# Optimization experiments

Hardware: AMD Instinct MI355X
Metric: run time of the kernel (lower is better)

The kernel has to match this reference:

```python
import jax, jax.numpy as jnp
import numpy as np

B, LQ, LK, D = 16, 1024, 4096, 256
SQRT_SCALE_INV = 0.25          # D ** -0.25, so scale = 1/sqrt(D)
HALF_BW = 128 // 2             # stripe_bandwdith // 2
NEG_INF = float('-inf')


def setup_inputs() -> dict:
    key = jax.random.key(0)
    k1, k2, k3, k4 = jax.random.split(key, 4)
    query = jax.random.normal(k1, (B, LQ, D), jnp.float32)
    key_t = jax.random.normal(k2, (B, LK, D), jnp.float32)
    value = jax.random.normal(k3, (B, LK, D), jnp.float32)
    # key lengths in [LK//2, LK]; masked_fill in torch requires max == LK
    key_lengths = jax.random.randint(k4, (B,), LK // 2, LK + 1).astype(jnp.int32)
    key_lengths = key_lengths.at[0].set(LK)
    query_lengths = jnp.full((B,), LQ, dtype=jnp.int32)  # full so no all-masked rows
    mask = jnp.arange(LK)[None, :] < key_lengths[:, None]  # [B, LK] bool, True = valid
    return {"query": query, "key": key_t, "value": value, "mask": mask,
            "query_lengths": query_lengths, "key_lengths": key_lengths}


def _stripe_mask(query_lengths, key_lengths, Lq, Lk):
    # band around line y = x * (key_len / query_len), per sample
    gx = jnp.arange(Lq, dtype=jnp.float32)[None, :, None]   # [1,Lq,1]
    gy = jnp.arange(Lk, dtype=jnp.float32)[None, None, :]   # [1,1,Lk]
    slope = (key_lengths.astype(jnp.float32) /
             query_lengths.astype(jnp.float32))[:, None, None]  # [B,1,1]
    center = gx * slope
    return (gy >= center - HALF_BW) & (gy <= center + HALF_BW)  # [B,Lq,Lk] bool


def reference(query, key, value, mask, query_lengths, key_lengths):
    # scores = (q * s) @ (k * s)^T  ==  (q @ k^T) * s^2
    scores = jnp.einsum('bqd,bkd->bqk', query, key) * (SQRT_SCALE_INV * SQRT_SCALE_INV)
    stripe = _stripe_mask(query_lengths, key_lengths, query.shape[1], key.shape[1])
    full_mask = mask[:, None, :] & stripe                    # padding AND stripe
    scores = jnp.where(full_mask, scores.astype(jnp.float32), NEG_INF)
    weight = jax.nn.softmax(scores, axis=-1).astype(query.dtype)
    # module applies no dropout (p=0) and returns (attn_weight, value)
    return (weight, value)
```

## Files before the change

### kernel.cpp

```cpp
#include <hip/hip_runtime.h>
#include <math.h>

constexpr int B_  = 16;
constexpr int LQ_ = 1024;
constexpr int LK_ = 4096;
constexpr int D_  = 256;
constexpr float HALF_BW_F = 64.0f;
constexpr float SCALE = 0.0625f;

typedef float  fx4    __attribute__((ext_vector_type(4)));
typedef short  bf16x8 __attribute__((ext_vector_type(8)));
typedef float  f32x4v __attribute__((ext_vector_type(4)));

constexpr int ROWS_PER_WAVE = 16;
constexpr int NUNIT = (B_ * LQ_) / ROWS_PER_WAVE;
constexpr int NXCD  = 8;
constexpr int UNIT_PER_XCD = NUNIT / NXCD;
constexpr int KSPAN = 192;
constexpr int NT    = 12;

__device__ __forceinline__ unsigned short f2bf(float f) {
    unsigned int u = __float_as_uint(f);
    return (unsigned short)((u + 0x7FFFu + ((u >> 16) & 1u)) >> 16);
}
__device__ __forceinline__ bf16x8 pack8(float4 a, float4 b) {
    bf16x8 r;
    r[0] = (short)f2bf(a.x); r[1] = (short)f2bf(a.y);
    r[2] = (short)f2bf(a.z); r[3] = (short)f2bf(a.w);
    r[4] = (short)f2bf(b.x); r[5] = (short)f2bf(b.y);
    r[6] = (short)f2bf(b.z); r[7] = (short)f2bf(b.w);
    return r;
}
__device__ __forceinline__ float grp16_max(float v) {
    #pragma unroll
    for (int off = 8; off > 0; off >>= 1)
        v = fmaxf(v, __shfl_xor(v, off, 64));
    return v;
}
__device__ __forceinline__ float grp16_sum(float v) {
    #pragma unroll
    for (int off = 8; off > 0; off >>= 1)
        v += __shfl_xor(v, off, 64);
    return v;
}

__global__ __launch_bounds__(64, 2) void fused_kernel(
    const float* __restrict__ Q, const float* __restrict__ K,
    const float* __restrict__ V,
    const int* __restrict__ qlen, const int* __restrict__ klen,
    float* __restrict__ Wout, float* __restrict__ Vout)
{
    const int Bid  = blockIdx.x;
    const int rb   = (Bid & (NXCD - 1)) * UNIT_PER_XCD + (Bid >> 3);
    const int lane = threadIdx.x;
    const int row0 = rb * ROWS_PER_WAVE;
    const int b    = row0 >> 10;
    const int qi0  = row0 & (LQ_ - 1);

    __shared__ float s_sc[ROWS_PER_WAVE][KSPAN];

    const int   key_len = klen[b];
    const float slope   = (float)key_len / (float)qlen[b];

    int lo_w = (int)ceilf((float)qi0 * slope - HALF_BW_F);
    if (lo_w < 0) lo_w = 0;
    int hi_w = (int)floorf((float)(qi0 + 15) * slope + HALF_BW_F);
    if (hi_w > key_len - 1) hi_w = key_len - 1;
    const int nt = (hi_w - lo_w) / 16 + 1;

    const int col = lane & 15;
    const int kg  = lane >> 4;

    const float* qb = Q + ((size_t)b * LQ_ + qi0 + col) * D_ + kg * 8;
    bf16x8 qf[8];
    #pragma unroll
    for (int kc = 0; kc < 8; ++kc) {
        const float4 u = *(const float4*)(qb + kc * 32);
        const float4 v = *(const float4*)(qb + kc * 32 + 4);
        qf[kc] = pack8(u, v);
    }

    const float* kb = K + (size_t)b * LK_ * D_ + kg * 8;
    f32x4v acc[NT];
    #pragma unroll
    for (int t = 0; t < NT; ++t) acc[t] = (f32x4v){0.f, 0.f, 0.f, 0.f};

    #pragma unroll
    for (int t = 0; t < NT; ++t) {
        if (t < nt) {
            const int key  = lo_w + t * 16 + col;
            const int keyc = (key <= hi_w) ? key : hi_w;
            const float* kp = kb + (size_t)keyc * D_;
            float4 u[8], w[8];
            #pragma unroll
            for (int kc = 0; kc < 8; ++kc) {
                u[kc] = *(const float4*)(kp + kc * 32);
                w[kc] = *(const float4*)(kp + kc * 32 + 4);
            }
            #pragma unroll
            for (int kc = 0; kc < 8; ++kc) {
                const bf16x8 kf = pack8(u[kc], w[kc]);
                acc[t] = __builtin_amdgcn_mfma_f32_16x16x32_bf16(qf[kc], kf, acc[t], 0, 0, 0);
            }
        }
    }

    #pragma unroll
    for (int r = 0; r < 4; ++r) {
        const int rg = kg * 4 + r;
        const float center = (float)(qi0 + rg) * slope;
        int klo = (int)ceilf(center - HALF_BW_F); if (klo < 0) klo = 0;
        int khi = (int)floorf(center + HALF_BW_F); if (khi > key_len - 1) khi = key_len - 1;

        float v[NT];
        #pragma unroll
        for (int t = 0; t < NT; ++t) {
            const int key = lo_w + t * 16 + col;
            v[t] = (t < nt && key >= klo && key <= khi) ? acc[t][r] * SCALE : -INFINITY;
        }
        float mx = v[0];
        #pragma unroll
        for (int t = 1; t < NT; ++t) mx = fmaxf(mx, v[t]);
        mx = grp16_max(mx);

        float e[NT], ssum = 0.f;
        #pragma unroll
        for (int t = 0; t < NT; ++t) { e[t] = __expf(v[t] - mx); ssum += e[t]; }
        ssum = grp16_sum(ssum);
        const float inv = 1.0f / ssum;

        #pragma unroll
        for (int t = 0; t < NT; ++t)
            if (t < nt) s_sc[rg][t * 16 + col] = e[t] * inv;
    }

    #pragma unroll
    for (int r = 0; r < 16; ++r) {
        const float center = (float)(qi0 + r) * slope;
        int klo = (int)ceilf(center - HALF_BW_F); if (klo < 0) klo = 0;
        int khi = (int)floorf(center + HALF_BW_F); if (khi > key_len - 1) khi = key_len - 1;
        const int s_lo = klo >> 8, s_hi = khi >> 8;
        float* base = Wout + (size_t)(row0 + r) * LK_;
        const float* sr = &s_sc[r][0];
        #pragma unroll
        for (int j = 0; j < 16; ++j) {
            const int c0 = (j * 64 + lane) * 4;
            float w[4] = {0.f, 0.f, 0.f, 0.f};
            if (j >= s_lo && j <= s_hi && c0 + 3 >= klo && c0 <= khi) {
                #pragma unroll
                for (int i = 0; i < 4; ++i) {
                    const int c = c0 + i;
                    if (c >= klo && c <= khi) w[i] = sr[c - lo_w];
                }
            }
            fx4 w4; w4.x = w[0]; w4.y = w[1]; w4.z = w[2]; w4.w = w[3];
            __builtin_nontemporal_store(w4, (fx4*)(base + c0));
        }
    }

    {
        const float* vs = V    + (size_t)row0 * 1024;
        float*       vd = Vout + (size_t)row0 * 1024;
        #pragma unroll
        for (int it = 0; it < 64; ++it) {
            const int o = (it * 64 + lane) * 4;
            fx4 t = __builtin_nontemporal_load((const fx4*)(vs + o));
            __builtin_nontemporal_store(t, (fx4*)(vd + o));
        }
    }
}

extern "C" void kernel_launch(void* const* d_in, const int* in_sizes, int n_in,
                              void* d_out, int out_size, void* d_ws, size_t ws_size,
                              hipStream_t stream) {
    const float* Q    = (const float*)d_in[0];
    const float* K    = (const float*)d_in[1];
    const float* V    = (const float*)d_in[2];
    const int*   qlen = (const int*)d_in[4];
    const int*   klen = (const int*)d_in[5];

    float* Wout = (float*)d_out;
    const size_t W_ELEMS = (size_t)B_ * LQ_ * LK_;
    float* Vout = Wout + W_ELEMS;

    fused_kernel<<<dim3(NUNIT), dim3(64), 0, stream>>>(
        Q, K, V, qlen, klen, Wout, Vout);
}
```

Baseline: 120.3 us.

## Split each 16-row unit across four waves with shared-memory softmax

Each block now has 256 threads instead of 64. The four waves each compute a third of the 12 key tiles of QK^T with MFMA and stage the raw scaled scores in shared memory. After a barrier, each wave runs the softmax and writes the weights for 4 of the 16 rows, and copies its own share of the V passthrough. The aim is more in-flight memory traffic per CU and less register pressure per wave than the single-wave-per-unit design. The cost is a block barrier, extra LDS traffic, and each wave reloading the same Q fragment.

```diff
diff --git a/kernel.cpp b/kernel.cpp
--- a/kernel.cpp
+++ b/kernel.cpp
@@ -12,12 +12,13 @@
 typedef short  bf16x8 __attribute__((ext_vector_type(8)));
 typedef float  f32x4v __attribute__((ext_vector_type(4)));
 
-constexpr int ROWS_PER_WAVE = 16;
-constexpr int NUNIT = (B_ * LQ_) / ROWS_PER_WAVE;
+constexpr int ROWS_PER_UNIT = 16;
+constexpr int NUNIT = (B_ * LQ_) / ROWS_PER_UNIT;
 constexpr int NXCD  = 8;
 constexpr int UNIT_PER_XCD = NUNIT / NXCD;
 constexpr int KSPAN = 192;
 constexpr int NT    = 12;
+constexpr int TPW   = 3;
 
 __device__ __forceinline__ unsigned short f2bf(float f) {
     unsigned int u = __float_as_uint(f);
@@ -31,33 +32,35 @@
     r[6] = (short)f2bf(b.z); r[7] = (short)f2bf(b.w);
     return r;
 }
-__device__ __forceinline__ float grp16_max(float v) {
+__device__ __forceinline__ float wave_max(float v) {
     #pragma unroll
-    for (int off = 8; off > 0; off >>= 1)
+    for (int off = 32; off > 0; off >>= 1)
         v = fmaxf(v, __shfl_xor(v, off, 64));
     return v;
 }
-__device__ __forceinline__ float grp16_sum(float v) {
+__device__ __forceinline__ float wave_sum(float v) {
     #pragma unroll
-    for (int off = 8; off > 0; off >>= 1)
+    for (int off = 32; off > 0; off >>= 1)
         v += __shfl_xor(v, off, 64);
     return v;
 }
 
-__global__ __launch_bounds__(64, 2) void fused_kernel(
+__global__ __launch_bounds__(256, 4) void fused_kernel(
     const float* __restrict__ Q, const float* __restrict__ K,
     const float* __restrict__ V,
     const int* __restrict__ qlen, const int* __restrict__ klen,
     float* __restrict__ Wout, float* __restrict__ Vout)
 {
     const int Bid  = blockIdx.x;
-    const int rb   = (Bid & (NXCD - 1)) * UNIT_PER_XCD + (Bid >> 3);
-    const int lane = threadIdx.x;
-    const int row0 = rb * ROWS_PER_WAVE;
+    const int unit = (Bid & (NXCD - 1)) * UNIT_PER_XCD + (Bid >> 3);
+    const int tid  = threadIdx.x;
+    const int lane = tid & 63;
+    const int wave = tid >> 6;
+    const int row0 = unit * ROWS_PER_UNIT;
     const int b    = row0 >> 10;
     const int qi0  = row0 & (LQ_ - 1);
 
-    __shared__ float s_sc[ROWS_PER_WAVE][KSPAN];
+    __shared__ float s_sc[ROWS_PER_UNIT][KSPAN];
 
     const int   key_len = klen[b];
     const float slope   = (float)key_len / (float)qlen[b];
@@ -81,12 +84,9 @@
     }
 
     const float* kb = K + (size_t)b * LK_ * D_ + kg * 8;
-    f32x4v acc[NT];
     #pragma unroll
-    for (int t = 0; t < NT; ++t) acc[t] = (f32x4v){0.f, 0.f, 0.f, 0.f};
-
-    #pragma unroll
-    for (int t = 0; t < NT; ++t) {
+    for (int s = 0; s < TPW; ++s) {
+        const int t = wave + 4 * s;
         if (t < nt) {
             const int key  = lo_w + t * 16 + col;
             const int keyc = (key <= hi_w) ? key : hi_w;
@@ -97,51 +97,47 @@
                 u[kc] = *(const float4*)(kp + kc * 32);
                 w[kc] = *(const float4*)(kp + kc * 32 + 4);
             }
+            f32x4v acc = (f32x4v){0.f, 0.f, 0.f, 0.f};
             #pragma unroll
             for (int kc = 0; kc < 8; ++kc) {
                 const bf16x8 kf = pack8(u[kc], w[kc]);
-                acc[t] = __builtin_amdgcn_mfma_f32_16x16x32_bf16(qf[kc], kf, acc[t], 0, 0, 0);
+                acc = __builtin_amdgcn_mfma_f32_16x16x32_bf16(qf[kc], kf, acc, 0, 0, 0);
             }
+            #pragma unroll
+            for (int r = 0; r < 4; ++r)
+                s_sc[kg * 4 + r][t * 16 + col] = acc[r] * SCALE;
         }
     }
+    __syncthreads();
 
     #pragma unroll
     for (int r = 0; r < 4; ++r) {
-        const int rg = kg * 4 + r;
+        const int rg = wave * 4 + r;
         const float center = (float)(qi0 + rg) * slope;
         int klo = (int)ceilf(center - HALF_BW_F); if (klo < 0) klo = 0;
         int khi = (int)floorf(center + HALF_BW_F); if (khi > key_len - 1) khi = key_len - 1;
 
-        float v[NT];
-        #pragma unroll
-        for (int t = 0; t < NT; ++t) {
-            const int key = lo_w + t * 16 + col;
-            v[t] = (t < nt && key >= klo && key <= khi) ? acc[t][r] * SCALE : -INFINITY;
+        float v0, v1, v2;
+        {
+            const int i0 = lane, i1 = lane + 64, i2 = lane + 128;
+            const int c0 = lo_w + i0, c1 = lo_w + i1, c2 = lo_w + i2;
+            v0 = (c0 >= klo && c0 <= khi) ? s_sc[rg][i0] : -INFINITY;
+            v1 = (c1 >= klo && c1 <= khi) ? s_sc[rg][i1] : -INFINITY;
+            v2 = (c2 >= klo && c2 <= khi) ? s_sc[rg][i2] : -INFINITY;
         }
-        float mx = v[0];
-        #pragma unroll
-        for (int t = 1; t < NT; ++t) mx = fmaxf(mx, v[t]);
-        mx = grp16_max(mx);
+        const float mx = wave_max(fmaxf(fmaxf(v0, v1), v2));
+        const float e0 = __expf(v0 - mx);
+        const float e1 = __expf(v1 - mx);
+        const float e2 = __expf(v2 - mx);
+        const float ssum = wave_sum(e0 + e1 + e2);
+        const float inv = 1.0f / ssum;
+        s_sc[rg][lane]       = e0 * inv;
+        s_sc[rg][lane + 64]  = e1 * inv;
+        s_sc[rg][lane + 128] = e2 * inv;
 
-        float e[NT], ssum = 0.f;
-        #pragma unroll
-        for (int t = 0; t < NT; ++t) { e[t] = __expf(v[t] - mx); ssum += e[t]; }
-        ssum = grp16_sum(ssum);
-        const float inv = 1.0f / ssum;
-
-        #pragma unroll
-        for (int t = 0; t < NT; ++t)
-            if (t < nt) s_sc[rg][t * 16 + col] = e[t] * inv;
-    }
-
-    #pragma unroll
-    for (int r = 0; r < 16; ++r) {
-        const float center = (float)(qi0 + r) * slope;
-        int klo = (int)ceilf(center - HALF_BW_F); if (klo < 0) klo = 0;
-        int khi = (int)floorf(center + HALF_BW_F); if (khi > key_len - 1) khi = key_len - 1;
         const int s_lo = klo >> 8, s_hi = khi >> 8;
-        float* base = Wout + (size_t)(row0 + r) * LK_;
-        const float* sr = &s_sc[r][0];
+        float* base = Wout + (size_t)(row0 + rg) * LK_;
+        const float* sr = &s_sc[rg][0];
         #pragma unroll
         for (int j = 0; j < 16; ++j) {
             const int c0 = (j * 64 + lane) * 4;
@@ -159,10 +155,10 @@
     }
 
     {
-        const float* vs = V    + (size_t)row0 * 1024;
-        float*       vd = Vout + (size_t)row0 * 1024;
+        const float* vs = V    + (size_t)(row0 + wave * 4) * 1024;
+        float*       vd = Vout + (size_t)(row0 + wave * 4) * 1024;
         #pragma unroll
-        for (int it = 0; it < 64; ++it) {
+        for (int it = 0; it < 16; ++it) {
             const int o = (it * 64 + lane) * 4;
             fx4 t = __builtin_nontemporal_load((const fx4*)(vs + o));
             __builtin_nontemporal_store(t, (fx4*)(vd + o));
@@ -183,6 +179,6 @@
     const size_t W_ELEMS = (size_t)B_ * LQ_ * LK_;
     float* Vout = Wout + W_ELEMS;
 
-    fused_kernel<<<dim3(NUNIT), dim3(64), 0, stream>>>(
+    fused_kernel<<<dim3(NUNIT), dim3(256), 0, stream>>>(
         Q, K, V, qlen, klen, Wout, Vout);
 }
```

Result: faster. 99.20 us (-17.6%).
